# Optimization experiments

Measured on AMD Instinct MI355X. Metric: run time of the kernel, lower is better.

## Reference

```python
import jax, jax.numpy as jnp
import numpy as np

REG_MAX = 16
TOPK = 13
ALPHA = 1.0
BETA = 6.0
MATCH_W = 0.5
IOU_W = 7.5
DFL_W = 1.5
EPS = 1e-7
NEG_INF = -1e30


def _iou(b1, b2):
    # xyxy IoU, broadcastable [..., 4]
    x1 = jnp.maximum(b1[..., 0], b2[..., 0]); y1 = jnp.maximum(b1[..., 1], b2[..., 1])
    x2 = jnp.minimum(b1[..., 2], b2[..., 2]); y2 = jnp.minimum(b1[..., 3], b2[..., 3])
    inter = jnp.maximum(x2 - x1, 0.0) * jnp.maximum(y2 - y1, 0.0)
    a1 = (b1[..., 2] - b1[..., 0]) * (b1[..., 3] - b1[..., 1])
    a2 = (b2[..., 2] - b2[..., 0]) * (b2[..., 3] - b2[..., 1])
    return inter / (a1 + a2 - inter + EPS)


def _ciou(b1, b2):
    iou = _iou(b1, b2)
    w1 = b1[..., 2] - b1[..., 0]; h1 = b1[..., 3] - b1[..., 1]
    w2 = b2[..., 2] - b2[..., 0]; h2 = b2[..., 3] - b2[..., 1]
    cw = jnp.maximum(b1[..., 2], b2[..., 2]) - jnp.minimum(b1[..., 0], b2[..., 0])
    ch = jnp.maximum(b1[..., 3], b2[..., 3]) - jnp.minimum(b1[..., 1], b2[..., 1])
    c2 = cw * cw + ch * ch + EPS
    rho2 = ((b2[..., 0] + b2[..., 2] - b1[..., 0] - b1[..., 2]) ** 2
            + (b2[..., 1] + b2[..., 3] - b1[..., 1] - b1[..., 3]) ** 2) / 4.0
    v = (4.0 / jnp.pi ** 2) * (jnp.arctan(w2 / (h2 + EPS)) - jnp.arctan(w1 / (h1 + EPS))) ** 2
    a = jax.lax.stop_gradient(v / (v - iou + (1.0 + EPS)))
    return iou - (rho2 / c2 + v * a)


def _per_sample(ps, pb, bd, gtb, gtl, vcm, anchor, stride):
    # ps [N,C], pb [N,4], bd [N,4*R], gtb [M,4], gtl [M], vcm [C] bool
    N, C = ps.shape
    M = gtb.shape[0]
    lab = jnp.clip(gtl, 0, C - 1)
    gt_valid = (gtl >= 0) & (gtl < C) & vcm[lab]
    ax, ay = anchor[:, 0], anchor[:, 1]
    inside = ((ax[None, :] >= gtb[:, 0:1]) & (ax[None, :] <= gtb[:, 2:3])
              & (ay[None, :] >= gtb[:, 1:2]) & (ay[None, :] <= gtb[:, 3:4]))  # [M,N]
    iou_mn = _iou(pb[None, :, :], gtb[:, None, :])                             # [M,N]
    cls_mn = jax.nn.sigmoid(ps[:, lab]).T                                      # [M,N]
    align = jnp.where(inside & gt_valid[:, None], cls_mn ** ALPHA * iou_mn ** BETA, NEG_INF)
    top_vals, top_idx = jax.lax.top_k(align, TOPK)                             # [M,K]
    cand = jnp.full((M, N), NEG_INF, ps.dtype).at[jnp.arange(M)[:, None], top_idx].set(top_vals)
    best = cand.max(0)          # final metric per anchor
    mg = cand.argmax(0)         # winning GT (first max == earliest GT, matching loop order)
    fg = best > -1.0            # align >= 0 always; non-candidates stay at NEG_INF
    m_lab = jnp.clip(gtl[mg], 0, C - 1)
    ov = iou_mn[mg, jnp.arange(N)]
    fgf = fg.astype(ps.dtype)
    tgt_scores = jax.nn.one_hot(m_lab, C, dtype=ps.dtype) * (jnp.maximum(ov, 0.1) * fgf)[:, None]
    tb = jnp.where(fg[:, None], gtb[mg], pb)   # safe target boxes (masked out when not fg)

    # classification BCE over valid classes (mean)
    bce = jnp.maximum(ps, 0.0) - ps * tgt_scores + jnp.log1p(jnp.exp(-jnp.abs(ps)))
    vc = vcm.astype(ps.dtype)
    match = (bce * vc[None, :]).sum() / (N * jnp.maximum(vc.sum(), 1.0))

    cnt = fg.sum()
    ciou_v = _ciou(pb, tb)
    iou_loss = jnp.where(cnt > 0, ((1.0 - ciou_v) * fgf).sum() / jnp.maximum(cnt, 1), 0.0)
    miou_sum = (_iou(pb, tb) * fgf).sum()
    probs = jax.nn.sigmoid(ps)
    pos_sum = (probs[jnp.arange(N), m_lab] * fgf).sum()

    # DFL
    d = jnp.concatenate([anchor - tb[:, :2], tb[:, 2:] - anchor], -1) / stride  # [N,4]
    d = jnp.clip(d, 0.0, REG_MAX - 1 - 0.01)
    tl = d.astype(jnp.int32)
    tr = jnp.minimum(tl + 1, REG_MAX - 1)
    wl = tr.astype(ps.dtype) - d
    wr = 1.0 - wl
    logp = jax.nn.log_softmax(bd.reshape(N, 4, REG_MAX), -1)
    ll = -jnp.take_along_axis(logp, tl[..., None], -1)[..., 0]
    lr = -jnp.take_along_axis(logp, tr[..., None], -1)[..., 0]
    dfl = jnp.where(cnt > 0, ((ll * wl + lr * wr) * fgf[:, None]).sum() / jnp.maximum(cnt * 4, 1), 0.0)

    mx = jnp.where(vcm[None, :], probs, NEG_INF).max(-1)
    neg_sum = (mx * (1.0 - fgf)).sum()
    neg_cnt = N - cnt
    return match, iou_loss, dfl, cnt, neg_cnt, pos_sum, neg_sum, miou_sum


def setup_inputs() -> dict:
    key = jax.random.key(0)
    B, N, C, M, R = 16, 8400, 80, 64, REG_MAX
    ks = jax.random.split(key, 7)
    pts, sts = [], []
    for s in (8, 16, 32):
        n = 640 // s
        g = (np.arange(n) + 0.5) * s
        xv, yv = np.meshgrid(g, g)
        pts.append(np.stack([xv.ravel(), yv.ravel()], 1))
        sts.append(np.full((n * n, 1), s, np.float32))
    anchor_points = jnp.asarray(np.concatenate(pts).astype(np.float32))  # [8400,2]
    stride_tensor = jnp.asarray(np.concatenate(sts))                      # [8400,1]
    c = anchor_points[None] + jax.random.normal(ks[0], (B, N, 2)) * stride_tensor[None]
    wh = jax.random.uniform(ks[1], (B, N, 2), minval=8.0, maxval=128.0)
    pred_boxes = jnp.concatenate([jnp.clip(c - wh / 2, 0.0, 640.0),
                                  jnp.clip(c + wh / 2, 0.0, 640.0)], -1)
    gc = jax.random.uniform(ks[2], (B, M, 2), minval=64.0, maxval=576.0)
    gwh = jax.random.uniform(ks[3], (B, M, 2), minval=16.0, maxval=128.0)
    gt_boxes = jnp.concatenate([gc - gwh / 2, gc + gwh / 2], -1)
    gt_labels = jax.random.randint(ks[4], (B, M), 0, C)
    class_mask = jnp.ones((B, C), bool)
    pred_scores = jax.random.normal(ks[5], (B, N, C))
    box_distribution = jax.random.normal(ks[6], (B, N, 4 * R))
    return {"pred_scores": pred_scores, "pred_boxes": pred_boxes,
            "anchor_points": anchor_points, "stride_tensor": stride_tensor,
            "box_distribution": box_distribution, "gt_boxes": gt_boxes,
            "gt_labels": gt_labels, "class_mask": class_mask}


def reference(pred_scores, pred_boxes, anchor_points, stride_tensor,
              box_distribution, gt_boxes, gt_labels, class_mask):
    B = pred_scores.shape[0]
    f = lambda ps, pb, bd, gtb, gtl, vcm: _per_sample(ps, pb, bd, gtb, gtl, vcm,
                                                      anchor_points, stride_tensor)
    match, iou_l, dfl, cnt, ncnt, psum, nsum, misum = jax.vmap(f)(
        pred_scores, pred_boxes, box_distribution, gt_boxes, gt_labels, class_mask)
    tot_pos = cnt.sum()
    tot_neg = ncnt.sum()
    total_match = match.sum(); total_iou = iou_l.sum(); total_dfl = dfl.sum()
    loss = (MATCH_W * total_match + IOU_W * total_iou + DFL_W * total_dfl) / B
    mean_pos = psum.sum() / jnp.maximum(tot_pos, 1)
    mean_neg = nsum.sum() / jnp.maximum(tot_neg, 1)
    mean_miou = misum.sum() / jnp.maximum(tot_pos, 1)
    return (loss, total_match / B, total_iou / B, total_dfl / B,
            tot_pos.astype(jnp.float32), mean_pos, mean_neg, mean_miou)
```

## Files before the change

### kernel.cpp

```cpp
#include <hip/hip_runtime.h>
#include <stdint.h>

#define TOPK 13
#define NEG_INF_F (-1e30f)
#define EPSF 1e-7f
#define L2EF 1.4426950408889634f
#define LN2F 0.6931471805599453f
#define MAXCAND 2048

__device__ __forceinline__ int mask_at(const uint8_t* __restrict__ raw, int i) {
    bool as_u8 = (raw[1] | raw[2] | raw[3]) != 0;
    return as_u8 ? (raw[i] != 0) : (((const int*)raw)[i] != 0);
}

__device__ __forceinline__ float iou_pair(float ax1, float ay1, float ax2, float ay2,
                                          float bx1, float by1, float bx2, float by2) {
    float x1 = fmaxf(ax1, bx1), y1 = fmaxf(ay1, by1);
    float x2 = fminf(ax2, bx2), y2 = fminf(ay2, by2);
    float inter = fmaxf(x2 - x1, 0.f) * fmaxf(y2 - y1, 0.f);
    float a1 = (ax2 - ax1) * (ay2 - ay1);
    float a2 = (bx2 - bx1) * (by2 - by1);
    return inter / (a1 + a2 - inter + EPSF);
}

__device__ __forceinline__ float sigmoid_fast(float s) {
    return 1.f / (1.f + exp2f(-s * L2EF));
}
__device__ __forceinline__ float softplus_bce(float s) {
    float t = exp2f(-fabsf(s) * L2EF);
    return fmaxf(s, 0.f) + log2f(1.f + t) * LN2F;
}

__device__ __forceinline__ void assign_wave(
    const float* __restrict__ ps, const float* __restrict__ pb,
    const float* __restrict__ gtb, const int* __restrict__ gtl,
    const uint8_t* __restrict__ mraw,
    unsigned long long* __restrict__ best, int B, int N, int C, int M,
    int t, int lane) {
    int b = t % B;
    int m = t / B;

    int lbl = gtl[b * M + m];
    int lab = min(max(lbl, 0), C - 1);
    if (!((lbl >= 0) && (lbl < C) && (mask_at(mraw, b * C + lab) != 0))) return;

    float4 g = ((const float4*)gtb)[(size_t)b * M + m];

    const int   n0_[3]  = { 0, 6400, 8000 };
    const int   dim_[3] = { 80, 40, 20 };
    const float sv_[3]  = { 8.f, 16.f, 32.f };

    int ix0[3], iy0[3], ww[3], pre[4];
    pre[0] = 0;
#pragma unroll
    for (int l = 0; l < 3; ++l) {
        float s = sv_[l]; int d = dim_[l];
        int ax0 = max(0,     (int)ceilf (g.x / s - 0.5f));
        int ax1 = min(d - 1, (int)floorf(g.z / s - 0.5f));
        int ay0 = max(0,     (int)ceilf (g.y / s - 0.5f));
        int ay1 = min(d - 1, (int)floorf(g.w / s - 0.5f));
        int w = max(0, ax1 - ax0 + 1);
        int h = max(0, ay1 - ay0 + 1);
        ix0[l] = ax0; iy0[l] = ay0; ww[l] = w;
        pre[l + 1] = pre[l] + w * h;
    }
    int tot = pre[3];
    if (tot == 0) return;

    const float* psb = ps + (size_t)b * N * C + lab;
    const float4* pbb = (const float4*)pb + (size_t)b * N;

    float lv[TOPK];
    int   li[TOPK];
#pragma unroll
    for (int j = 0; j < TOPK; ++j) { lv[j] = NEG_INF_F; li[j] = -1; }

    for (int tt = lane; tt < tot; tt += 64) {
        int l = (tt >= pre[1]) + (tt >= pre[2]);
        int r = tt - pre[l];
        int w = ww[l];
        int iy = r / w, ix = r - iy * w;
        int gx = ix0[l] + ix, gy = iy0[l] + iy;
        int n = n0_[l] + gy * dim_[l] + gx;
        float4 p = pbb[n];
        float iou = iou_pair(p.x, p.y, p.z, p.w, g.x, g.y, g.z, g.w);
        float sc = psb[(size_t)n * C];
        float i3 = iou * iou * iou;
        float val = sigmoid_fast(sc) * i3 * i3;
        if (val > lv[TOPK - 1]) {
            bool placed = false;
#pragma unroll
            for (int j = TOPK - 1; j >= 1; --j) {
                if (!placed) {
                    if (val > lv[j - 1]) { lv[j] = lv[j - 1]; li[j] = li[j - 1]; }
                    else { lv[j] = val; li[j] = n; placed = true; }
                }
            }
            if (!placed) { lv[0] = val; li[0] = n; }
        }
    }

    unsigned key = 0xFFFFFFFFu - (unsigned)m;
    unsigned long long* bb = best + (size_t)b * N;
    int rounds = min(tot, TOPK);
    for (int p = 0; p < rounds; ++p) {
        float bv = lv[0]; int bn = li[0];
        for (int off = 32; off > 0; off >>= 1) {
            float ov = __shfl_down(bv, off, 64);
            int   on = __shfl_down(bn, off, 64);
            if (ov > bv || (ov == bv && (unsigned)on < (unsigned)bn)) { bv = ov; bn = on; }
        }
        bv = __shfl(bv, 0, 64);
        bn = __shfl(bn, 0, 64);
        if (bn < 0) break;
        if (li[0] == bn) {
            unsigned long long pk =
                ((unsigned long long)__float_as_uint(lv[0]) << 32) | (unsigned long long)key;
            atomicMax(bb + bn, pk);
#pragma unroll
            for (int j = 0; j < TOPK - 1; ++j) { lv[j] = lv[j + 1]; li[j] = li[j + 1]; }
            lv[TOPK - 1] = NEG_INF_F; li[TOPK - 1] = -1;
        }
    }
}

__global__ __launch_bounds__(256, 1) void fused_a_k(
    const float* __restrict__ ps, const float* __restrict__ pb,
    const float* __restrict__ gtb, const int* __restrict__ gtl,
    const uint8_t* __restrict__ mraw,
    unsigned long long* __restrict__ best, float* __restrict__ smaxbuf,
    float* __restrict__ partials, int B, int N, int C, int M,
    int asgb, int nb) {
    if ((int)blockIdx.x < asgb) {
        int t = blockIdx.x * 4 + (threadIdx.x >> 6);
        if (t < B * M)
            assign_wave(ps, pb, gtb, gtl, mraw, best, B, N, C, M, t, threadIdx.x & 63);
        return;
    }
    int bi = blockIdx.x - asgb;
    int b = bi / nb;
    int n = (bi % nb) * 256 + threadIdx.x;

    __shared__ int smask[256];
    __shared__ int s_notall;
    __shared__ float sredA[4];
    if (threadIdx.x == 0) s_notall = 0;
    __syncthreads();
    for (int c = threadIdx.x; c < C && c < 256; c += 256) {
        int v = mask_at(mraw, b * C + c);
        smask[c] = v;
        if (!v) s_notall = 1;
    }
    __syncthreads();
    bool allm = (s_notall == 0);

    float acc0 = 0.f;
    if (n < N) {
        const float* psr = ps + ((size_t)b * N + n) * C;
        float bce_sum = 0.f, smax = NEG_INF_F;

        if (C == 80 && allm) {
            const float4* p4 = (const float4*)psr;
            float4 s4[20];
#pragma unroll
            for (int i = 0; i < 20; ++i) s4[i] = p4[i];
#pragma unroll
            for (int i = 0; i < 20; ++i) {
                bce_sum += softplus_bce(s4[i].x) + softplus_bce(s4[i].y) +
                           softplus_bce(s4[i].z) + softplus_bce(s4[i].w);
                smax = fmaxf(smax, fmaxf(fmaxf(s4[i].x, s4[i].y), fmaxf(s4[i].z, s4[i].w)));
            }
        } else if (allm) {
            int c4 = C & ~3;
            for (int c = 0; c < c4; c += 4) {
                float4 s4 = *(const float4*)(psr + c);
                bce_sum += softplus_bce(s4.x) + softplus_bce(s4.y) +
                           softplus_bce(s4.z) + softplus_bce(s4.w);
                smax = fmaxf(smax, fmaxf(fmaxf(s4.x, s4.y), fmaxf(s4.z, s4.w)));
            }
            for (int c = c4; c < C; ++c) {
                float s = psr[c];
                bce_sum += softplus_bce(s);
                smax = fmaxf(smax, s);
            }
        } else {
            for (int c = 0; c < C; ++c) {
                float s = psr[c];
                if (smask[c]) { bce_sum += softplus_bce(s); smax = fmaxf(smax, s); }
            }
        }
        smaxbuf[(size_t)b * N + n] = smax;
        acc0 = bce_sum;
    }

    int lane = threadIdx.x & 63, wid = threadIdx.x >> 6;
    float v = acc0;
    for (int off = 32; off > 0; off >>= 1) v += __shfl_down(v, off, 64);
    if (lane == 0) sredA[wid] = v;
    __syncthreads();
    if (threadIdx.x == 0)
        atomicAdd(&partials[b * 8 + 0], sredA[0] + sredA[1] + sredA[2] + sredA[3]);
}

__global__ __launch_bounds__(256, 1) void fused_b_k(
    const float* __restrict__ ps, const float* __restrict__ pb,
    const float* __restrict__ anch, const float* __restrict__ strd,
    const float* __restrict__ bd, const float* __restrict__ gtb,
    const int* __restrict__ gtl, const uint8_t* __restrict__ mraw,
    const unsigned long long* __restrict__ best, const float* __restrict__ smaxbuf,
    float* __restrict__ partials, unsigned int* __restrict__ done_ctr,
    float* __restrict__ out, int B, int N, int C, int M) {
    int b = blockIdx.y;
    int n = blockIdx.x * 256 + threadIdx.x;

    __shared__ float sred[4 * 8];
    __shared__ int s_last;

    float acc0 = 0, acc1 = 0, acc2 = 0, acc3 = 0, acc4 = 0, acc5 = 0, acc6 = 0;

    if (n < N) {
        unsigned long long pk = best[(size_t)b * N + n];
        bool fg = (pk != 0ull);
        float smax = smaxbuf[(size_t)b * N + n];
        acc1 = fg ? 1.f : 0.f;
        acc3 = fg ? 0.f : sigmoid_fast(smax);

        if (fg) {
            int mg = (int)(0xFFFFFFFFu - (unsigned)(pk & 0xFFFFFFFFull));
            int lbl = gtl[b * M + mg];
            int m_lab = min(max(lbl, 0), C - 1);

            const float* bdr = bd + ((size_t)b * N + n) * 64;
            const float4* bq4 = (const float4*)bdr;
            float4 bq[16];
#pragma unroll
            for (int i = 0; i < 16; ++i) bq[i] = bq4[i];
            float4 p = ((const float4*)pb)[(size_t)b * N + n];
            float4 g = ((const float4*)gtb)[(size_t)b * M + mg];
            float2 an = ((const float2*)anch)[n];
            float stv = strd[n];
            float slab = ps[((size_t)b * N + n) * C + m_lab];

            float ov = iou_pair(p.x, p.y, p.z, p.w, g.x, g.y, g.z, g.w);
            acc0 = -fmaxf(ov, 0.1f) * slab;
            acc2 = sigmoid_fast(slab);
            acc4 = ov;
            float w1 = p.z - p.x, h1 = p.w - p.y;
            float w2 = g.z - g.x, h2 = g.w - g.y;
            float cw = fmaxf(p.z, g.z) - fminf(p.x, g.x);
            float ch = fmaxf(p.w, g.w) - fminf(p.y, g.y);
            float c2 = cw * cw + ch * ch + EPSF;
            float dx = g.x + g.z - p.x - p.z;
            float dy = g.y + g.w - p.y - p.w;
            float rho2 = (dx * dx + dy * dy) * 0.25f;
            const float PI = 3.14159265358979323846f;
            float dv = atanf(w2 / (h2 + EPSF)) - atanf(w1 / (h1 + EPSF));
            float v = (4.f / (PI * PI)) * dv * dv;
            float a = v / (v - ov + 1.f + EPSF);
            acc5 = 1.f - (ov - (rho2 / c2 + v * a));
            float dall[4] = { (an.x - g.x) / stv, (an.y - g.y) / stv,
                              (g.z - an.x) / stv, (g.w - an.y) / stv };
            float dfl = 0.f;
#pragma unroll
            for (int k = 0; k < 4; ++k) {
                float4 q0 = bq[k * 4 + 0], q1 = bq[k * 4 + 1];
                float4 q2 = bq[k * 4 + 2], q3 = bq[k * 4 + 3];
                float mxv = fmaxf(fmaxf(fmaxf(q0.x, q0.y), fmaxf(q0.z, q0.w)),
                                  fmaxf(fmaxf(q1.x, q1.y), fmaxf(q1.z, q1.w)));
                mxv = fmaxf(mxv, fmaxf(fmaxf(fmaxf(q2.x, q2.y), fmaxf(q2.z, q2.w)),
                                        fmaxf(fmaxf(q3.x, q3.y), fmaxf(q3.z, q3.w))));
                float se = exp2f((q0.x - mxv) * L2EF) + exp2f((q0.y - mxv) * L2EF) +
                           exp2f((q0.z - mxv) * L2EF) + exp2f((q0.w - mxv) * L2EF) +
                           exp2f((q1.x - mxv) * L2EF) + exp2f((q1.y - mxv) * L2EF) +
                           exp2f((q1.z - mxv) * L2EF) + exp2f((q1.w - mxv) * L2EF) +
                           exp2f((q2.x - mxv) * L2EF) + exp2f((q2.y - mxv) * L2EF) +
                           exp2f((q2.z - mxv) * L2EF) + exp2f((q2.w - mxv) * L2EF) +
                           exp2f((q3.x - mxv) * L2EF) + exp2f((q3.y - mxv) * L2EF) +
                           exp2f((q3.z - mxv) * L2EF) + exp2f((q3.w - mxv) * L2EF);
                float lse = mxv + log2f(se) * LN2F;
                float d = fminf(fmaxf(dall[k], 0.f), 14.99f);
                int tl = (int)d;
                int tr = min(tl + 1, 15);
                float wl = (float)tr - d;
                float xtl = bdr[k * 16 + tl];
                float xtr = bdr[k * 16 + tr];
                dfl += (lse - xtl) * wl + (lse - xtr) * (1.f - wl);
            }
            acc6 = dfl;
        }
    }

    int lane = threadIdx.x & 63, wid = threadIdx.x >> 6;
    float accs[7] = { acc0, acc1, acc2, acc3, acc4, acc5, acc6 };
#pragma unroll
    for (int j = 0; j < 7; ++j) {
        float v = accs[j];
        for (int off = 32; off > 0; off >>= 1) v += __shfl_down(v, off, 64);
        if (lane == 0) sred[wid * 8 + j] = v;
    }
    __syncthreads();
    if (threadIdx.x < 7) {
        float s = sred[0 * 8 + threadIdx.x] + sred[1 * 8 + threadIdx.x] +
                  sred[2 * 8 + threadIdx.x] + sred[3 * 8 + threadIdx.x];
        atomicAdd(&partials[b * 8 + threadIdx.x], s);
    }
    __syncthreads();

    if (threadIdx.x == 0) {
        __threadfence();
        unsigned r = atomicAdd(done_ctr, 1u);
        s_last = (r == gridDim.x * gridDim.y - 1u) ? 1 : 0;
    }
    __syncthreads();
    if (!s_last) return;
    if (threadIdx.x >= 64) return;
    __threadfence();

    int fl = threadIdx.x;
    float tm = 0, ti = 0, td = 0, tp = 0, tneg = 0, pos = 0, neg = 0, miou = 0;
    for (int s = fl; s < B; s += 64) {
        float vcs = 0.f;
        for (int c = 0; c < C; ++c) vcs += mask_at(mraw, s * C + c) ? 1.f : 0.f;
        const float* pr = partials + s * 8;
        float p0 = __hip_atomic_load(&pr[0], __ATOMIC_RELAXED, __HIP_MEMORY_SCOPE_AGENT);
        float p1 = __hip_atomic_load(&pr[1], __ATOMIC_RELAXED, __HIP_MEMORY_SCOPE_AGENT);
        float p2 = __hip_atomic_load(&pr[2], __ATOMIC_RELAXED, __HIP_MEMORY_SCOPE_AGENT);
        float p3 = __hip_atomic_load(&pr[3], __ATOMIC_RELAXED, __HIP_MEMORY_SCOPE_AGENT);
        float p4 = __hip_atomic_load(&pr[4], __ATOMIC_RELAXED, __HIP_MEMORY_SCOPE_AGENT);
        float p5 = __hip_atomic_load(&pr[5], __ATOMIC_RELAXED, __HIP_MEMORY_SCOPE_AGENT);
        float p6 = __hip_atomic_load(&pr[6], __ATOMIC_RELAXED, __HIP_MEMORY_SCOPE_AGENT);
        float cnt = p1;
        tm += p0 / ((float)N * fmaxf(vcs, 1.f));
        ti += (cnt > 0.f) ? p5 / fmaxf(cnt, 1.f) : 0.f;
        td += (cnt > 0.f) ? p6 / fmaxf(cnt * 4.f, 1.f) : 0.f;
        tp += cnt; tneg += (float)N - cnt;
        pos += p2; neg += p3; miou += p4;
    }
    for (int off = 32; off > 0; off >>= 1) {
        tm += __shfl_down(tm, off, 64);   ti += __shfl_down(ti, off, 64);
        td += __shfl_down(td, off, 64);   tp += __shfl_down(tp, off, 64);
        tneg += __shfl_down(tneg, off, 64); pos += __shfl_down(pos, off, 64);
        neg += __shfl_down(neg, off, 64); miou += __shfl_down(miou, off, 64);
    }
    if (fl == 0) {
        float Bf = (float)B;
        out[0] = (0.5f * tm + 7.5f * ti + 1.5f * td) / Bf;
        out[1] = tm / Bf;
        out[2] = ti / Bf;
        out[3] = td / Bf;
        out[4] = tp;
        out[5] = pos / fmaxf(tp, 1.f);
        out[6] = neg / fmaxf(tneg, 1.f);
        out[7] = miou / fmaxf(tp, 1.f);
    }
}

__global__ __launch_bounds__(256) void assign_topk_k(
    const float* __restrict__ ps, const float* __restrict__ pb,
    const float* __restrict__ anch, const float* __restrict__ gtb,
    const int* __restrict__ gtl, const uint8_t* __restrict__ mraw,
    unsigned long long* __restrict__ best, int B, int N, int C, int M) {
    int b = blockIdx.x % B;
    int m = blockIdx.x / B;

    __shared__ float cval[MAXCAND];
    __shared__ int   cidx[MAXCAND];
    __shared__ int   scnt;
    if (threadIdx.x == 0) scnt = 0;

    int lbl = gtl[b * M + m];
    int lab = min(max(lbl, 0), C - 1);
    bool valid = (lbl >= 0) && (lbl < C) && (mask_at(mraw, b * C + lab) != 0);
    __syncthreads();

    if (valid) {
        float4 g = ((const float4*)gtb)[(size_t)b * M + m];
        const float* psb = ps + (size_t)b * N * C + lab;
        const float4* pbb = (const float4*)pb + (size_t)b * N;
        for (int n = threadIdx.x; n < N; n += 256) {
            float2 a = ((const float2*)anch)[n];
            if (a.x < g.x || a.x > g.z || a.y < g.y || a.y > g.w) continue;
            float4 p = pbb[n];
            float iou = iou_pair(p.x, p.y, p.z, p.w, g.x, g.y, g.z, g.w);
            float s = psb[(size_t)n * C];
            float i3 = iou * iou * iou;
            float val = sigmoid_fast(s) * i3 * i3;
            int slot = atomicAdd(&scnt, 1);
            if (slot < MAXCAND) { cval[slot] = val; cidx[slot] = n; }
        }
    }
    __syncthreads();
    if (!valid || threadIdx.x >= 64) return;

    int total = min(scnt, MAXCAND);
    if (total == 0) return;
    int lane = threadIdx.x;

    float lv[TOPK];
    int   li[TOPK];
#pragma unroll
    for (int j = 0; j < TOPK; ++j) { lv[j] = NEG_INF_F; li[j] = -1; }
    for (int i = lane; i < total; i += 64) {
        float v = cval[i]; int ix = cidx[i];
        if (v > lv[TOPK - 1]) {
            bool placed = false;
#pragma unroll
            for (int j = TOPK - 1; j >= 1; --j) {
                if (!placed) {
                    if (v > lv[j - 1]) { lv[j] = lv[j - 1]; li[j] = li[j - 1]; }
                    else { lv[j] = v; li[j] = ix; placed = true; }
                }
            }
            if (!placed) { lv[0] = v; li[0] = ix; }
        }
    }

    unsigned key = 0xFFFFFFFFu - (unsigned)m;
    unsigned long long* bb = best + (size_t)b * N;
    int rounds = min(total, TOPK);
    for (int p = 0; p < rounds; ++p) {
        float bv = lv[0]; int bn = li[0];
        for (int off = 32; off > 0; off >>= 1) {
            float ov = __shfl_down(bv, off, 64);
            int   on = __shfl_down(bn, off, 64);
            if (ov > bv || (ov == bv && (unsigned)on < (unsigned)bn)) { bv = ov; bn = on; }
        }
        bv = __shfl(bv, 0, 64);
        bn = __shfl(bn, 0, 64);
        if (bn < 0) break;
        if (li[0] == bn) {
            unsigned long long pk =
                ((unsigned long long)__float_as_uint(lv[0]) << 32) | (unsigned long long)key;
            atomicMax(bb + bn, pk);
#pragma unroll
            for (int j = 0; j < TOPK - 1; ++j) { lv[j] = lv[j + 1]; li[j] = li[j + 1]; }
            lv[TOPK - 1] = NEG_INF_F; li[TOPK - 1] = -1;
        }
    }
}

__global__ __launch_bounds__(256, 1) void per_anchor_k(
    const float* __restrict__ ps, const float* __restrict__ pb,
    const float* __restrict__ anch, const float* __restrict__ strd,
    const float* __restrict__ bd, const float* __restrict__ gtb,
    const int* __restrict__ gtl, const uint8_t* __restrict__ mraw,
    const unsigned long long* __restrict__ best,
    float* __restrict__ partials, int B, int N, int C, int M) {
    int b = blockIdx.y;
    int n = blockIdx.x * 256 + threadIdx.x;

    __shared__ int smask[256];
    __shared__ int s_notall;
    __shared__ float sred[4 * 8];
    if (threadIdx.x == 0) s_notall = 0;
    __syncthreads();
    for (int c = threadIdx.x; c < C && c < 256; c += 256) {
        int v = mask_at(mraw, b * C + c);
        smask[c] = v;
        if (!v) s_notall = 1;
    }
    __syncthreads();
    bool allm = (s_notall == 0);

    float acc0 = 0, acc1 = 0, acc2 = 0, acc3 = 0, acc4 = 0, acc5 = 0, acc6 = 0;

    if (n < N) {
        unsigned long long pk = best[(size_t)b * N + n];
        bool fg = (pk != 0ull);
        int mg = fg ? (int)(0xFFFFFFFFu - (unsigned)(pk & 0xFFFFFFFFull)) : 0;
        int lbl = gtl[b * M + mg];
        int m_lab = min(max(lbl, 0), C - 1);

        const float* psr = ps + ((size_t)b * N + n) * C;
        float bce_sum = 0.f, smax = NEG_INF_F;

        if (C == 80 && allm) {
            const float4* p4 = (const float4*)psr;
            float4 s4[20];
#pragma unroll
            for (int i = 0; i < 20; ++i) s4[i] = p4[i];
#pragma unroll
            for (int i = 0; i < 20; ++i) {
                bce_sum += softplus_bce(s4[i].x) + softplus_bce(s4[i].y) +
                           softplus_bce(s4[i].z) + softplus_bce(s4[i].w);
                smax = fmaxf(smax, fmaxf(fmaxf(s4[i].x, s4[i].y), fmaxf(s4[i].z, s4[i].w)));
            }
        } else if (allm) {
            int c4 = C & ~3;
            for (int c = 0; c < c4; c += 4) {
                float4 s4 = *(const float4*)(psr + c);
                bce_sum += softplus_bce(s4.x) + softplus_bce(s4.y) +
                           softplus_bce(s4.z) + softplus_bce(s4.w);
                smax = fmaxf(smax, fmaxf(fmaxf(s4.x, s4.y), fmaxf(s4.z, s4.w)));
            }
            for (int c = c4; c < C; ++c) {
                float s = psr[c];
                bce_sum += softplus_bce(s);
                smax = fmaxf(smax, s);
            }
        } else {
            for (int c = 0; c < C; ++c) {
                float s = psr[c];
                if (smask[c]) { bce_sum += softplus_bce(s); smax = fmaxf(smax, s); }
            }
        }

        acc1 = fg ? 1.f : 0.f;
        acc3 = fg ? 0.f : sigmoid_fast(smax);

        if (fg) {
            const float* bdr = bd + ((size_t)b * N + n) * 64;
            const float4* bq4 = (const float4*)bdr;
            float4 bq[16];
#pragma unroll
            for (int i = 0; i < 16; ++i) bq[i] = bq4[i];
            float4 p = ((const float4*)pb)[(size_t)b * N + n];
            float4 g = ((const float4*)gtb)[(size_t)b * M + mg];
            float2 an = ((const float2*)anch)[n];
            float stv = strd[n];
            float slab = psr[m_lab];

            float ov = iou_pair(p.x, p.y, p.z, p.w, g.x, g.y, g.z, g.w);
            bce_sum -= fmaxf(ov, 0.1f) * slab;
            acc2 = sigmoid_fast(slab);
            acc4 = ov;
            float w1 = p.z - p.x, h1 = p.w - p.y;
            float w2 = g.z - g.x, h2 = g.w - g.y;
            float cw = fmaxf(p.z, g.z) - fminf(p.x, g.x);
            float ch = fmaxf(p.w, g.w) - fminf(p.y, g.y);
            float c2 = cw * cw + ch * ch + EPSF;
            float dx = g.x + g.z - p.x - p.z;
            float dy = g.y + g.w - p.y - p.w;
            float rho2 = (dx * dx + dy * dy) * 0.25f;
            const float PI = 3.14159265358979323846f;
            float dv = atanf(w2 / (h2 + EPSF)) - atanf(w1 / (h1 + EPSF));
            float v = (4.f / (PI * PI)) * dv * dv;
            float a = v / (v - ov + 1.f + EPSF);
            acc5 = 1.f - (ov - (rho2 / c2 + v * a));
            float dall[4] = { (an.x - g.x) / stv, (an.y - g.y) / stv,
                              (g.z - an.x) / stv, (g.w - an.y) / stv };
            float dfl = 0.f;
#pragma unroll
            for (int k = 0; k < 4; ++k) {
                float4 q0 = bq[k * 4 + 0], q1 = bq[k * 4 + 1];
                float4 q2 = bq[k * 4 + 2], q3 = bq[k * 4 + 3];
                float mxv = fmaxf(fmaxf(fmaxf(q0.x, q0.y), fmaxf(q0.z, q0.w)),
                                  fmaxf(fmaxf(q1.x, q1.y), fmaxf(q1.z, q1.w)));
                mxv = fmaxf(mxv, fmaxf(fmaxf(fmaxf(q2.x, q2.y), fmaxf(q2.z, q2.w)),
                                        fmaxf(fmaxf(q3.x, q3.y), fmaxf(q3.z, q3.w))));
                float se = exp2f((q0.x - mxv) * L2EF) + exp2f((q0.y - mxv) * L2EF) +
                           exp2f((q0.z - mxv) * L2EF) + exp2f((q0.w - mxv) * L2EF) +
                           exp2f((q1.x - mxv) * L2EF) + exp2f((q1.y - mxv) * L2EF) +
                           exp2f((q1.z - mxv) * L2EF) + exp2f((q1.w - mxv) * L2EF) +
                           exp2f((q2.x - mxv) * L2EF) + exp2f((q2.y - mxv) * L2EF) +
                           exp2f((q2.z - mxv) * L2EF) + exp2f((q2.w - mxv) * L2EF) +
                           exp2f((q3.x - mxv) * L2EF) + exp2f((q3.y - mxv) * L2EF) +
                           exp2f((q3.z - mxv) * L2EF) + exp2f((q3.w - mxv) * L2EF);
                float lse = mxv + log2f(se) * LN2F;
                float d = fminf(fmaxf(dall[k], 0.f), 14.99f);
                int tl = (int)d;
                int tr = min(tl + 1, 15);
                float wl = (float)tr - d;
                float xtl = bdr[k * 16 + tl];
                float xtr = bdr[k * 16 + tr];
                dfl += (lse - xtl) * wl + (lse - xtr) * (1.f - wl);
            }
            acc6 = dfl;
        }
        acc0 = bce_sum;
    }

    int lane = threadIdx.x & 63, wid = threadIdx.x >> 6;
    float accs[7] = { acc0, acc1, acc2, acc3, acc4, acc5, acc6 };
#pragma unroll
    for (int j = 0; j < 7; ++j) {
        float v = accs[j];
        for (int off = 32; off > 0; off >>= 1) v += __shfl_down(v, off, 64);
        if (lane == 0) sred[wid * 8 + j] = v;
    }
    __syncthreads();
    if (threadIdx.x < 7) {
        float s = sred[0 * 8 + threadIdx.x] + sred[1 * 8 + threadIdx.x] +
                  sred[2 * 8 + threadIdx.x] + sred[3 * 8 + threadIdx.x];
        atomicAdd(&partials[b * 8 + threadIdx.x], s);
    }
}

__global__ void finalize_k(const float* __restrict__ partials, const uint8_t* __restrict__ mraw,
                           float* __restrict__ out, int B, int N, int C) {
    int lane = threadIdx.x;
    float tm = 0, ti = 0, td = 0, tp = 0, tneg = 0, pos = 0, neg = 0, miou = 0;
    if (lane < B) {
        float vcs = 0.f;
        for (int c = 0; c < C; ++c) vcs += mask_at(mraw, lane * C + c) ? 1.f : 0.f;
        const float* pr = partials + lane * 8;
        float cnt = pr[1];
        tm = pr[0] / ((float)N * fmaxf(vcs, 1.f));
        ti = (cnt > 0.f) ? pr[5] / fmaxf(cnt, 1.f) : 0.f;
        td = (cnt > 0.f) ? pr[6] / fmaxf(cnt * 4.f, 1.f) : 0.f;
        tp = cnt; tneg = (float)N - cnt;
        pos = pr[2]; neg = pr[3]; miou = pr[4];
    }
    for (int off = 32; off > 0; off >>= 1) {
        tm += __shfl_down(tm, off, 64);   ti += __shfl_down(ti, off, 64);
        td += __shfl_down(td, off, 64);   tp += __shfl_down(tp, off, 64);
        tneg += __shfl_down(tneg, off, 64); pos += __shfl_down(pos, off, 64);
        neg += __shfl_down(neg, off, 64); miou += __shfl_down(miou, off, 64);
    }
    if (lane == 0) {
        float Bf = (float)B;
        out[0] = (0.5f * tm + 7.5f * ti + 1.5f * td) / Bf;
        out[1] = tm / Bf;
        out[2] = ti / Bf;
        out[3] = td / Bf;
        out[4] = tp;
        out[5] = pos / fmaxf(tp, 1.f);
        out[6] = neg / fmaxf(tneg, 1.f);
        out[7] = miou / fmaxf(tp, 1.f);
    }
}

extern "C" void kernel_launch(void* const* d_in, const int* in_sizes, int n_in,
                              void* d_out, int out_size, void* d_ws, size_t ws_size,
                              hipStream_t stream) {
    const float* ps   = (const float*)d_in[0];
    const float* pb   = (const float*)d_in[1];
    const float* anch = (const float*)d_in[2];
    const float* strd = (const float*)d_in[3];
    const float* bd   = (const float*)d_in[4];
    const float* gtb  = (const float*)d_in[5];
    const int*   gtl  = (const int*)d_in[6];
    const uint8_t* cmsk = (const uint8_t*)d_in[7];

    int N = in_sizes[2] / 2;
    int B = in_sizes[1] / (4 * N);
    int C = in_sizes[0] / (B * N);
    int M = in_sizes[6] / B;

    size_t bestBytes = (size_t)B * N * sizeof(unsigned long long);
    size_t off1 = (bestBytes + 255) & ~(size_t)255;
    size_t partBytes = (size_t)B * 8 * sizeof(float);
    size_t off2 = (off1 + partBytes + 255) & ~(size_t)255;
    size_t zeroBytes = off2 + 256;
    unsigned long long* best = (unsigned long long*)d_ws;
    float* partials = (float*)((char*)d_ws + off1);
    unsigned int* done_ctr = (unsigned int*)((char*)d_ws + off2);
    float* smaxbuf = (float*)((char*)d_ws + zeroBytes);

    hipMemsetAsync(d_ws, 0, zeroBytes, stream);

    int nb = (N + 255) / 256;
    if (N == 8400) {
        int asgb = (B * M + 3) / 4;
        fused_a_k<<<asgb + B * nb, 256, 0, stream>>>(ps, pb, gtb, gtl, cmsk,
                                                     best, smaxbuf, partials,
                                                     B, N, C, M, asgb, nb);
        fused_b_k<<<dim3(nb, B), 256, 0, stream>>>(ps, pb, anch, strd, bd, gtb, gtl, cmsk,
                                                   best, smaxbuf, partials, done_ctr,
                                                   (float*)d_out, B, N, C, M);
    } else {
        assign_topk_k<<<B * M, 256, 0, stream>>>(ps, pb, anch, gtb, gtl, cmsk, best, B, N, C, M);
        dim3 gB(nb, B);
        per_anchor_k<<<gB, 256, 0, stream>>>(ps, pb, anch, strd, bd, gtb, gtl, cmsk, best,
                                             partials, B, N, C, M);
        finalize_k<<<1, 64, 0, stream>>>(partials, cmsk, (float*)d_out, B, N, C);
    }
}
```

Baseline: 155.4 us.

## Compact foreground anchors into a list and process only those in second pass

During top-k assignment, the first atomicMax that claims a new anchor also appends it to a global compacted list. The second kernel then runs only over the listed foreground anchors instead of over every anchor. The negative-score sigmoid sum moves into the first kernel, which now writes sigmoid values instead of raw maxima; the second kernel subtracts them for foreground anchors. Per-block partials are accumulated in LDS atomics before going to global memory, at the cost of extra contended global atomics in the assign phase and a list-ordering dependence on atomic timing.

```diff
diff --git a/kernel.cpp b/kernel.cpp
--- a/kernel.cpp
+++ b/kernel.cpp
@@ -7,6 +7,7 @@
 #define L2EF 1.4426950408889634f
 #define LN2F 0.6931471805599453f
 #define MAXCAND 2048
+#define MAXB_LDS 64
 
 __device__ __forceinline__ int mask_at(const uint8_t* __restrict__ raw, int i) {
     bool as_u8 = (raw[1] | raw[2] | raw[3]) != 0;
@@ -35,8 +36,9 @@
     const float* __restrict__ ps, const float* __restrict__ pb,
     const float* __restrict__ gtb, const int* __restrict__ gtl,
     const uint8_t* __restrict__ mraw,
-    unsigned long long* __restrict__ best, int B, int N, int C, int M,
-    int t, int lane) {
+    unsigned long long* __restrict__ best,
+    unsigned* __restrict__ list, unsigned* __restrict__ list_cnt,
+    int B, int N, int C, int M, int t, int lane) {
     int b = t % B;
     int m = t / B;
 
@@ -116,7 +118,11 @@
         if (li[0] == bn) {
             unsigned long long pk =
                 ((unsigned long long)__float_as_uint(lv[0]) << 32) | (unsigned long long)key;
-            atomicMax(bb + bn, pk);
+            unsigned long long old = atomicMax(bb + bn, pk);
+            if (old == 0ull) {
+                unsigned slot = atomicAdd(list_cnt, 1u);
+                list[slot] = ((unsigned)b << 16) | (unsigned)bn;
+            }
 #pragma unroll
             for (int j = 0; j < TOPK - 1; ++j) { lv[j] = lv[j + 1]; li[j] = li[j + 1]; }
             lv[TOPK - 1] = NEG_INF_F; li[TOPK - 1] = -1;
@@ -128,13 +134,15 @@
     const float* __restrict__ ps, const float* __restrict__ pb,
     const float* __restrict__ gtb, const int* __restrict__ gtl,
     const uint8_t* __restrict__ mraw,
-    unsigned long long* __restrict__ best, float* __restrict__ smaxbuf,
-    float* __restrict__ partials, int B, int N, int C, int M,
-    int asgb, int nb) {
+    unsigned long long* __restrict__ best,
+    unsigned* __restrict__ list, unsigned* __restrict__ list_cnt,
+    float* __restrict__ sigbuf, float* __restrict__ partials,
+    int B, int N, int C, int M, int asgb, int nb) {
     if ((int)blockIdx.x < asgb) {
         int t = blockIdx.x * 4 + (threadIdx.x >> 6);
         if (t < B * M)
-            assign_wave(ps, pb, gtb, gtl, mraw, best, B, N, C, M, t, threadIdx.x & 63);
+            assign_wave(ps, pb, gtb, gtl, mraw, best, list, list_cnt,
+                        B, N, C, M, t, threadIdx.x & 63);
         return;
     }
     int bi = blockIdx.x - asgb;
@@ -143,7 +151,7 @@
 
     __shared__ int smask[256];
     __shared__ int s_notall;
-    __shared__ float sredA[4];
+    __shared__ float sredA[4], sredB[4];
     if (threadIdx.x == 0) s_notall = 0;
     __syncthreads();
     for (int c = threadIdx.x; c < C && c < 256; c += 256) {
@@ -154,7 +162,7 @@
     __syncthreads();
     bool allm = (s_notall == 0);
 
-    float acc0 = 0.f;
+    float acc0 = 0.f, acc3 = 0.f;
     if (n < N) {
         const float* psr = ps + ((size_t)b * N + n) * C;
         float bce_sum = 0.f, smax = NEG_INF_F;
@@ -189,17 +197,24 @@
                 if (smask[c]) { bce_sum += softplus_bce(s); smax = fmaxf(smax, s); }
             }
         }
-        smaxbuf[(size_t)b * N + n] = smax;
+        float sg = sigmoid_fast(smax);
+        sigbuf[(size_t)b * N + n] = sg;
         acc0 = bce_sum;
+        acc3 = sg;
     }
 
     int lane = threadIdx.x & 63, wid = threadIdx.x >> 6;
-    float v = acc0;
-    for (int off = 32; off > 0; off >>= 1) v += __shfl_down(v, off, 64);
-    if (lane == 0) sredA[wid] = v;
-    __syncthreads();
-    if (threadIdx.x == 0)
+    float v0 = acc0, v3 = acc3;
+    for (int off = 32; off > 0; off >>= 1) {
+        v0 += __shfl_down(v0, off, 64);
+        v3 += __shfl_down(v3, off, 64);
+    }
+    if (lane == 0) { sredA[wid] = v0; sredB[wid] = v3; }
+    __syncthreads();
+    if (threadIdx.x == 0) {
         atomicAdd(&partials[b * 8 + 0], sredA[0] + sredA[1] + sredA[2] + sredA[3]);
+        atomicAdd(&partials[b * 8 + 3], sredB[0] + sredB[1] + sredB[2] + sredB[3]);
+    }
 }
 
 __global__ __launch_bounds__(256, 1) void fused_b_k(
@@ -207,29 +222,302 @@
     const float* __restrict__ anch, const float* __restrict__ strd,
     const float* __restrict__ bd, const float* __restrict__ gtb,
     const int* __restrict__ gtl, const uint8_t* __restrict__ mraw,
-    const unsigned long long* __restrict__ best, const float* __restrict__ smaxbuf,
+    const unsigned long long* __restrict__ best, const float* __restrict__ sigbuf,
+    const unsigned* __restrict__ list, const unsigned* __restrict__ list_cnt,
     float* __restrict__ partials, unsigned int* __restrict__ done_ctr,
     float* __restrict__ out, int B, int N, int C, int M) {
+    __shared__ float sacc[MAXB_LDS * 8];
+    __shared__ int s_last;
+    bool use_lds = (B <= MAXB_LDS);
+    if (use_lds)
+        for (int i = threadIdx.x; i < B * 8; i += 256) sacc[i] = 0.f;
+    __syncthreads();
+
+    int cnt = (int)*list_cnt;
+    int idx = blockIdx.x * 256 + threadIdx.x;
+    if (idx < cnt) {
+        unsigned e = list[idx];
+        int b = (int)(e >> 16), n = (int)(e & 0xFFFFu);
+        unsigned long long pk = best[(size_t)b * N + n];
+        int mg = (int)(0xFFFFFFFFu - (unsigned)(pk & 0xFFFFFFFFull));
+        int lbl = gtl[b * M + mg];
+        int m_lab = min(max(lbl, 0), C - 1);
+
+        const float* bdr = bd + ((size_t)b * N + n) * 64;
+        const float4* bq4 = (const float4*)bdr;
+        float4 bq[16];
+#pragma unroll
+        for (int i = 0; i < 16; ++i) bq[i] = bq4[i];
+        float4 p = ((const float4*)pb)[(size_t)b * N + n];
+        float4 g = ((const float4*)gtb)[(size_t)b * M + mg];
+        float2 an = ((const float2*)anch)[n];
+        float stv = strd[n];
+        float slab = ps[((size_t)b * N + n) * C + m_lab];
+        float sg = sigbuf[(size_t)b * N + n];
+
+        float ov = iou_pair(p.x, p.y, p.z, p.w, g.x, g.y, g.z, g.w);
+        float acc0 = -fmaxf(ov, 0.1f) * slab;
+        float acc2 = sigmoid_fast(slab);
+        float acc4 = ov;
+        float w1 = p.z - p.x, h1 = p.w - p.y;
+        float w2 = g.z - g.x, h2 = g.w - g.y;
+        float cw = fmaxf(p.z, g.z) - fminf(p.x, g.x);
+        float ch = fmaxf(p.w, g.w) - fminf(p.y, g.y);
+        float c2 = cw * cw + ch * ch + EPSF;
+        float dx = g.x + g.z - p.x - p.z;
+        float dy = g.y + g.w - p.y - p.w;
+        float rho2 = (dx * dx + dy * dy) * 0.25f;
+        const float PI = 3.14159265358979323846f;
+        float dv = atanf(w2 / (h2 + EPSF)) - atanf(w1 / (h1 + EPSF));
+        float v = (4.f / (PI * PI)) * dv * dv;
+        float a = v / (v - ov + 1.f + EPSF);
+        float acc5 = 1.f - (ov - (rho2 / c2 + v * a));
+        float dall[4] = { (an.x - g.x) / stv, (an.y - g.y) / stv,
+                          (g.z - an.x) / stv, (g.w - an.y) / stv };
+        float dfl = 0.f;
+#pragma unroll
+        for (int k = 0; k < 4; ++k) {
+            float4 q0 = bq[k * 4 + 0], q1 = bq[k * 4 + 1];
+            float4 q2 = bq[k * 4 + 2], q3 = bq[k * 4 + 3];
+            float mxv = fmaxf(fmaxf(fmaxf(q0.x, q0.y), fmaxf(q0.z, q0.w)),
+                              fmaxf(fmaxf(q1.x, q1.y), fmaxf(q1.z, q1.w)));
+            mxv = fmaxf(mxv, fmaxf(fmaxf(fmaxf(q2.x, q2.y), fmaxf(q2.z, q2.w)),
+                                    fmaxf(fmaxf(q3.x, q3.y), fmaxf(q3.z, q3.w))));
+            float se = exp2f((q0.x - mxv) * L2EF) + exp2f((q0.y - mxv) * L2EF) +
+                       exp2f((q0.z - mxv) * L2EF) + exp2f((q0.w - mxv) * L2EF) +
+                       exp2f((q1.x - mxv) * L2EF) + exp2f((q1.y - mxv) * L2EF) +
+                       exp2f((q1.z - mxv) * L2EF) + exp2f((q1.w - mxv) * L2EF) +
+                       exp2f((q2.x - mxv) * L2EF) + exp2f((q2.y - mxv) * L2EF) +
+                       exp2f((q2.z - mxv) * L2EF) + exp2f((q2.w - mxv) * L2EF) +
+                       exp2f((q3.x - mxv) * L2EF) + exp2f((q3.y - mxv) * L2EF) +
+                       exp2f((q3.z - mxv) * L2EF) + exp2f((q3.w - mxv) * L2EF);
+            float lse = mxv + log2f(se) * LN2F;
+            float d = fminf(fmaxf(dall[k], 0.f), 14.99f);
+            int tl = (int)d;
+            int tr = min(tl + 1, 15);
+            float wl = (float)tr - d;
+            float xtl = bdr[k * 16 + tl];
+            float xtr = bdr[k * 16 + tr];
+            dfl += (lse - xtl) * wl + (lse - xtr) * (1.f - wl);
+        }
+        float accs[7] = { acc0, 1.f, acc2, -sg, acc4, acc5, dfl };
+        if (use_lds) {
+#pragma unroll
+            for (int j = 0; j < 7; ++j) atomicAdd(&sacc[b * 8 + j], accs[j]);
+        } else {
+#pragma unroll
+            for (int j = 0; j < 7; ++j) atomicAdd(&partials[b * 8 + j], accs[j]);
+        }
+    }
+    __syncthreads();
+    if (use_lds)
+        for (int i = threadIdx.x; i < B * 8; i += 256)
+            if (sacc[i] != 0.f) atomicAdd(&partials[i], sacc[i]);
+    __syncthreads();
+
+    if (threadIdx.x == 0) {
+        __threadfence();
+        unsigned r = atomicAdd(done_ctr, 1u);
+        s_last = (r == gridDim.x - 1u) ? 1 : 0;
+    }
+    __syncthreads();
+    if (!s_last) return;
+    if (threadIdx.x >= 64) return;
+    __threadfence();
+
+    int fl = threadIdx.x;
+    float tm = 0, ti = 0, td = 0, tp = 0, tneg = 0, pos = 0, neg = 0, miou = 0;
+    for (int s = fl; s < B; s += 64) {
+        float vcs = 0.f;
+        for (int c = 0; c < C; ++c) vcs += mask_at(mraw, s * C + c) ? 1.f : 0.f;
+        const float* pr = partials + s * 8;
+        float p0 = __hip_atomic_load(&pr[0], __ATOMIC_RELAXED, __HIP_MEMORY_SCOPE_AGENT);
+        float p1 = __hip_atomic_load(&pr[1], __ATOMIC_RELAXED, __HIP_MEMORY_SCOPE_AGENT);
+        float p2 = __hip_atomic_load(&pr[2], __ATOMIC_RELAXED, __HIP_MEMORY_SCOPE_AGENT);
+        float p3 = __hip_atomic_load(&pr[3], __ATOMIC_RELAXED, __HIP_MEMORY_SCOPE_AGENT);
+        float p4 = __hip_atomic_load(&pr[4], __ATOMIC_RELAXED, __HIP_MEMORY_SCOPE_AGENT);
+        float p5 = __hip_atomic_load(&pr[5], __ATOMIC_RELAXED, __HIP_MEMORY_SCOPE_AGENT);
+        float p6 = __hip_atomic_load(&pr[6], __ATOMIC_RELAXED, __HIP_MEMORY_SCOPE_AGENT);
+        float cnt = p1;
+        tm += p0 / ((float)N * fmaxf(vcs, 1.f));
+        ti += (cnt > 0.f) ? p5 / fmaxf(cnt, 1.f) : 0.f;
+        td += (cnt > 0.f) ? p6 / fmaxf(cnt * 4.f, 1.f) : 0.f;
+        tp += cnt; tneg += (float)N - cnt;
+        pos += p2; neg += p3; miou += p4;
+    }
+    for (int off = 32; off > 0; off >>= 1) {
+        tm += __shfl_down(tm, off, 64);   ti += __shfl_down(ti, off, 64);
+        td += __shfl_down(td, off, 64);   tp += __shfl_down(tp, off, 64);
+        tneg += __shfl_down(tneg, off, 64); pos += __shfl_down(pos, off, 64);
+        neg += __shfl_down(neg, off, 64); miou += __shfl_down(miou, off, 64);
+    }
+    if (fl == 0) {
+        float Bf = (float)B;
+        out[0] = (0.5f * tm + 7.5f * ti + 1.5f * td) / Bf;
+        out[1] = tm / Bf;
+        out[2] = ti / Bf;
+        out[3] = td / Bf;
+        out[4] = tp;
+        out[5] = pos / fmaxf(tp, 1.f);
+        out[6] = neg / fmaxf(tneg, 1.f);
+        out[7] = miou / fmaxf(tp, 1.f);
+    }
+}
+
+__global__ __launch_bounds__(256) void assign_topk_k(
+    const float* __restrict__ ps, const float* __restrict__ pb,
+    const float* __restrict__ anch, const float* __restrict__ gtb,
+    const int* __restrict__ gtl, const uint8_t* __restrict__ mraw,
+    unsigned long long* __restrict__ best, int B, int N, int C, int M) {
+    int b = blockIdx.x % B;
+    int m = blockIdx.x / B;
+
+    __shared__ float cval[MAXCAND];
+    __shared__ int   cidx[MAXCAND];
+    __shared__ int   scnt;
+    if (threadIdx.x == 0) scnt = 0;
+
+    int lbl = gtl[b * M + m];
+    int lab = min(max(lbl, 0), C - 1);
+    bool valid = (lbl >= 0) && (lbl < C) && (mask_at(mraw, b * C + lab) != 0);
+    __syncthreads();
+
+    if (valid) {
+        float4 g = ((const float4*)gtb)[(size_t)b * M + m];
+        const float* psb = ps + (size_t)b * N * C + lab;
+        const float4* pbb = (const float4*)pb + (size_t)b * N;
+        for (int n = threadIdx.x; n < N; n += 256) {
+            float2 a = ((const float2*)anch)[n];
+            if (a.x < g.x || a.x > g.z || a.y < g.y || a.y > g.w) continue;
+            float4 p = pbb[n];
+            float iou = iou_pair(p.x, p.y, p.z, p.w, g.x, g.y, g.z, g.w);
+            float s = psb[(size_t)n * C];
+            float i3 = iou * iou * iou;
+            float val = sigmoid_fast(s) * i3 * i3;
+            int slot = atomicAdd(&scnt, 1);
+            if (slot < MAXCAND) { cval[slot] = val; cidx[slot] = n; }
+        }
+    }
+    __syncthreads();
+    if (!valid || threadIdx.x >= 64) return;
+
+    int total = min(scnt, MAXCAND);
+    if (total == 0) return;
+    int lane = threadIdx.x;
+
+    float lv[TOPK];
+    int   li[TOPK];
+#pragma unroll
+    for (int j = 0; j < TOPK; ++j) { lv[j] = NEG_INF_F; li[j] = -1; }
+    for (int i = lane; i < total; i += 64) {
+        float v = cval[i]; int ix = cidx[i];
+        if (v > lv[TOPK - 1]) {
+            bool placed = false;
+#pragma unroll
+            for (int j = TOPK - 1; j >= 1; --j) {
+                if (!placed) {
+                    if (v > lv[j - 1]) { lv[j] = lv[j - 1]; li[j] = li[j - 1]; }
+                    else { lv[j] = v; li[j] = ix; placed = true; }
+                }
+            }
+            if (!placed) { lv[0] = v; li[0] = ix; }
+        }
+    }
+
+    unsigned key = 0xFFFFFFFFu - (unsigned)m;
+    unsigned long long* bb = best + (size_t)b * N;
+    int rounds = min(total, TOPK);
+    for (int p = 0; p < rounds; ++p) {
+        float bv = lv[0]; int bn = li[0];
+        for (int off = 32; off > 0; off >>= 1) {
+            float ov = __shfl_down(bv, off, 64);
+            int   on = __shfl_down(bn, off, 64);
+            if (ov > bv || (ov == bv && (unsigned)on < (unsigned)bn)) { bv = ov; bn = on; }
+        }
+        bv = __shfl(bv, 0, 64);
+        bn = __shfl(bn, 0, 64);
+        if (bn < 0) break;
+        if (li[0] == bn) {
+            unsigned long long pk =
+                ((unsigned long long)__float_as_uint(lv[0]) << 32) | (unsigned long long)key;
+            atomicMax(bb + bn, pk);
+#pragma unroll
+            for (int j = 0; j < TOPK - 1; ++j) { lv[j] = lv[j + 1]; li[j] = li[j + 1]; }
+            lv[TOPK - 1] = NEG_INF_F; li[TOPK - 1] = -1;
+        }
+    }
+}
+
+__global__ __launch_bounds__(256, 1) void per_anchor_k(
+    const float* __restrict__ ps, const float* __restrict__ pb,
+    const float* __restrict__ anch, const float* __restrict__ strd,
+    const float* __restrict__ bd, const float* __restrict__ gtb,
+    const int* __restrict__ gtl, const uint8_t* __restrict__ mraw,
+    const unsigned long long* __restrict__ best,
+    float* __restrict__ partials, int B, int N, int C, int M) {
     int b = blockIdx.y;
     int n = blockIdx.x * 256 + threadIdx.x;
 
+    __shared__ int smask[256];
+    __shared__ int s_notall;
     __shared__ float sred[4 * 8];
-    __shared__ int s_last;
+    if (threadIdx.x == 0) s_notall = 0;
+    __syncthreads();
+    for (int c = threadIdx.x; c < C && c < 256; c += 256) {
+        int v = mask_at(mraw, b * C + c);
+        smask[c] = v;
+        if (!v) s_notall = 1;
+    }
+    __syncthreads();
+    bool allm = (s_notall == 0);
 
     float acc0 = 0, acc1 = 0, acc2 = 0, acc3 = 0, acc4 = 0, acc5 = 0, acc6 = 0;
 
     if (n < N) {
         unsigned long long pk = best[(size_t)b * N + n];
         bool fg = (pk != 0ull);
-        float smax = smaxbuf[(size_t)b * N + n];
+        int mg = fg ? (int)(0xFFFFFFFFu - (unsigned)(pk & 0xFFFFFFFFull)) : 0;
+        int lbl = gtl[b * M + mg];
+        int m_lab = min(max(lbl, 0), C - 1);
+
+        const float* psr = ps + ((size_t)b * N + n) * C;
+        float bce_sum = 0.f, smax = NEG_INF_F;
+
+        if (C == 80 && allm) {
+            const float4* p4 = (const float4*)psr;
+            float4 s4[20];
+#pragma unroll
+            for (int i = 0; i < 20; ++i) s4[i] = p4[i];
+#pragma unroll
+            for (int i = 0; i < 20; ++i) {
+                bce_sum += softplus_bce(s4[i].x) + softplus_bce(s4[i].y) +
+                           softplus_bce(s4[i].z) + softplus_bce(s4[i].w);
+                smax = fmaxf(smax, fmaxf(fmaxf(s4[i].x, s4[i].y), fmaxf(s4[i].z, s4[i].w)));
+            }
+        } else if (allm) {
+            int c4 = C & ~3;
+            for (int c = 0; c < c4; c += 4) {
+                float4 s4 = *(const float4*)(psr + c);
+                bce_sum += softplus_bce(s4.x) + softplus_bce(s4.y) +
+                           softplus_bce(s4.z) + softplus_bce(s4.w);
+                smax = fmaxf(smax, fmaxf(fmaxf(s4.x, s4.y), fmaxf(s4.z, s4.w)));
+            }
+            for (int c = c4; c < C; ++c) {
+                float s = psr[c];
+                bce_sum += softplus_bce(s);
+                smax = fmaxf(smax, s);
+            }
+        } else {
+            for (int c = 0; c < C; ++c) {
+                float s = psr[c];
+                if (smask[c]) { bce_sum += softplus_bce(s); smax = fmaxf(smax, s); }
+            }
+        }
+
         acc1 = fg ? 1.f : 0.f;
         acc3 = fg ? 0.f : sigmoid_fast(smax);
 
         if (fg) {
-            int mg = (int)(0xFFFFFFFFu - (unsigned)(pk & 0xFFFFFFFFull));
-            int lbl = gtl[b * M + mg];
-            int m_lab = min(max(lbl, 0), C - 1);
-
             const float* bdr = bd + ((size_t)b * N + n) * 64;
             const float4* bq4 = (const float4*)bdr;
             float4 bq[16];
@@ -239,10 +527,10 @@
             float4 g = ((const float4*)gtb)[(size_t)b * M + mg];
             float2 an = ((const float2*)anch)[n];
             float stv = strd[n];
-            float slab = ps[((size_t)b * N + n) * C + m_lab];
+            float slab = psr[m_lab];
 
             float ov = iou_pair(p.x, p.y, p.z, p.w, g.x, g.y, g.z, g.w);
-            acc0 = -fmaxf(ov, 0.1f) * slab;
+            bce_sum -= fmaxf(ov, 0.1f) * slab;
             acc2 = sigmoid_fast(slab);
             acc4 = ov;
             float w1 = p.z - p.x, h1 = p.w - p.y;
@@ -288,285 +576,6 @@
             }
             acc6 = dfl;
         }
-    }
-
-    int lane = threadIdx.x & 63, wid = threadIdx.x >> 6;
-    float accs[7] = { acc0, acc1, acc2, acc3, acc4, acc5, acc6 };
-#pragma unroll
-    for (int j = 0; j < 7; ++j) {
-        float v = accs[j];
-        for (int off = 32; off > 0; off >>= 1) v += __shfl_down(v, off, 64);
-        if (lane == 0) sred[wid * 8 + j] = v;
-    }
-    __syncthreads();
-    if (threadIdx.x < 7) {
-        float s = sred[0 * 8 + threadIdx.x] + sred[1 * 8 + threadIdx.x] +
-                  sred[2 * 8 + threadIdx.x] + sred[3 * 8 + threadIdx.x];
-        atomicAdd(&partials[b * 8 + threadIdx.x], s);
-    }
-    __syncthreads();
-
-    if (threadIdx.x == 0) {
-        __threadfence();
-        unsigned r = atomicAdd(done_ctr, 1u);
-        s_last = (r == gridDim.x * gridDim.y - 1u) ? 1 : 0;
-    }
-    __syncthreads();
-    if (!s_last) return;
-    if (threadIdx.x >= 64) return;
-    __threadfence();
-
-    int fl = threadIdx.x;
-    float tm = 0, ti = 0, td = 0, tp = 0, tneg = 0, pos = 0, neg = 0, miou = 0;
-    for (int s = fl; s < B; s += 64) {
-        float vcs = 0.f;
-        for (int c = 0; c < C; ++c) vcs += mask_at(mraw, s * C + c) ? 1.f : 0.f;
-        const float* pr = partials + s * 8;
-        float p0 = __hip_atomic_load(&pr[0], __ATOMIC_RELAXED, __HIP_MEMORY_SCOPE_AGENT);
-        float p1 = __hip_atomic_load(&pr[1], __ATOMIC_RELAXED, __HIP_MEMORY_SCOPE_AGENT);
-        float p2 = __hip_atomic_load(&pr[2], __ATOMIC_RELAXED, __HIP_MEMORY_SCOPE_AGENT);
-        float p3 = __hip_atomic_load(&pr[3], __ATOMIC_RELAXED, __HIP_MEMORY_SCOPE_AGENT);
-        float p4 = __hip_atomic_load(&pr[4], __ATOMIC_RELAXED, __HIP_MEMORY_SCOPE_AGENT);
-        float p5 = __hip_atomic_load(&pr[5], __ATOMIC_RELAXED, __HIP_MEMORY_SCOPE_AGENT);
-        float p6 = __hip_atomic_load(&pr[6], __ATOMIC_RELAXED, __HIP_MEMORY_SCOPE_AGENT);
-        float cnt = p1;
-        tm += p0 / ((float)N * fmaxf(vcs, 1.f));
-        ti += (cnt > 0.f) ? p5 / fmaxf(cnt, 1.f) : 0.f;
-        td += (cnt > 0.f) ? p6 / fmaxf(cnt * 4.f, 1.f) : 0.f;
-        tp += cnt; tneg += (float)N - cnt;
-        pos += p2; neg += p3; miou += p4;
-    }
-    for (int off = 32; off > 0; off >>= 1) {
-        tm += __shfl_down(tm, off, 64);   ti += __shfl_down(ti, off, 64);
-        td += __shfl_down(td, off, 64);   tp += __shfl_down(tp, off, 64);
-        tneg += __shfl_down(tneg, off, 64); pos += __shfl_down(pos, off, 64);
-        neg += __shfl_down(neg, off, 64); miou += __shfl_down(miou, off, 64);
-    }
-    if (fl == 0) {
-        float Bf = (float)B;
-        out[0] = (0.5f * tm + 7.5f * ti + 1.5f * td) / Bf;
-        out[1] = tm / Bf;
-        out[2] = ti / Bf;
-        out[3] = td / Bf;
-        out[4] = tp;
-        out[5] = pos / fmaxf(tp, 1.f);
-        out[6] = neg / fmaxf(tneg, 1.f);
-        out[7] = miou / fmaxf(tp, 1.f);
-    }
-}
-
-__global__ __launch_bounds__(256) void assign_topk_k(
-    const float* __restrict__ ps, const float* __restrict__ pb,
-    const float* __restrict__ anch, const float* __restrict__ gtb,
-    const int* __restrict__ gtl, const uint8_t* __restrict__ mraw,
-    unsigned long long* __restrict__ best, int B, int N, int C, int M) {
-    int b = blockIdx.x % B;
-    int m = blockIdx.x / B;
-
-    __shared__ float cval[MAXCAND];
-    __shared__ int   cidx[MAXCAND];
-    __shared__ int   scnt;
-    if (threadIdx.x == 0) scnt = 0;
-
-    int lbl = gtl[b * M + m];
-    int lab = min(max(lbl, 0), C - 1);
-    bool valid = (lbl >= 0) && (lbl < C) && (mask_at(mraw, b * C + lab) != 0);
-    __syncthreads();
-
-    if (valid) {
-        float4 g = ((const float4*)gtb)[(size_t)b * M + m];
-        const float* psb = ps + (size_t)b * N * C + lab;
-        const float4* pbb = (const float4*)pb + (size_t)b * N;
-        for (int n = threadIdx.x; n < N; n += 256) {
-            float2 a = ((const float2*)anch)[n];
-            if (a.x < g.x || a.x > g.z || a.y < g.y || a.y > g.w) continue;
-            float4 p = pbb[n];
-            float iou = iou_pair(p.x, p.y, p.z, p.w, g.x, g.y, g.z, g.w);
-            float s = psb[(size_t)n * C];
-            float i3 = iou * iou * iou;
-            float val = sigmoid_fast(s) * i3 * i3;
-            int slot = atomicAdd(&scnt, 1);
-            if (slot < MAXCAND) { cval[slot] = val; cidx[slot] = n; }
-        }
-    }
-    __syncthreads();
-    if (!valid || threadIdx.x >= 64) return;
-
-    int total = min(scnt, MAXCAND);
-    if (total == 0) return;
-    int lane = threadIdx.x;
-
-    float lv[TOPK];
-    int   li[TOPK];
-#pragma unroll
-    for (int j = 0; j < TOPK; ++j) { lv[j] = NEG_INF_F; li[j] = -1; }
-    for (int i = lane; i < total; i += 64) {
-        float v = cval[i]; int ix = cidx[i];
-        if (v > lv[TOPK - 1]) {
-            bool placed = false;
-#pragma unroll
-            for (int j = TOPK - 1; j >= 1; --j) {
-                if (!placed) {
-                    if (v > lv[j - 1]) { lv[j] = lv[j - 1]; li[j] = li[j - 1]; }
-                    else { lv[j] = v; li[j] = ix; placed = true; }
-                }
-            }
-            if (!placed) { lv[0] = v; li[0] = ix; }
-        }
-    }
-
-    unsigned key = 0xFFFFFFFFu - (unsigned)m;
-    unsigned long long* bb = best + (size_t)b * N;
-    int rounds = min(total, TOPK);
-    for (int p = 0; p < rounds; ++p) {
-        float bv = lv[0]; int bn = li[0];
-        for (int off = 32; off > 0; off >>= 1) {
-            float ov = __shfl_down(bv, off, 64);
-            int   on = __shfl_down(bn, off, 64);
-            if (ov > bv || (ov == bv && (unsigned)on < (unsigned)bn)) { bv = ov; bn = on; }
-        }
-        bv = __shfl(bv, 0, 64);
-        bn = __shfl(bn, 0, 64);
-        if (bn < 0) break;
-        if (li[0] == bn) {
-            unsigned long long pk =
-                ((unsigned long long)__float_as_uint(lv[0]) << 32) | (unsigned long long)key;
-            atomicMax(bb + bn, pk);
-#pragma unroll
-            for (int j = 0; j < TOPK - 1; ++j) { lv[j] = lv[j + 1]; li[j] = li[j + 1]; }
-            lv[TOPK - 1] = NEG_INF_F; li[TOPK - 1] = -1;
-        }
-    }
-}
-
-__global__ __launch_bounds__(256, 1) void per_anchor_k(
-    const float* __restrict__ ps, const float* __restrict__ pb,
-    const float* __restrict__ anch, const float* __restrict__ strd,
-    const float* __restrict__ bd, const float* __restrict__ gtb,
-    const int* __restrict__ gtl, const uint8_t* __restrict__ mraw,
-    const unsigned long long* __restrict__ best,
-    float* __restrict__ partials, int B, int N, int C, int M) {
-    int b = blockIdx.y;
-    int n = blockIdx.x * 256 + threadIdx.x;
-
-    __shared__ int smask[256];
-    __shared__ int s_notall;
-    __shared__ float sred[4 * 8];
-    if (threadIdx.x == 0) s_notall = 0;
-    __syncthreads();
-    for (int c = threadIdx.x; c < C && c < 256; c += 256) {
-        int v = mask_at(mraw, b * C + c);
-        smask[c] = v;
-        if (!v) s_notall = 1;
-    }
-    __syncthreads();
-    bool allm = (s_notall == 0);
-
-    float acc0 = 0, acc1 = 0, acc2 = 0, acc3 = 0, acc4 = 0, acc5 = 0, acc6 = 0;
-
-    if (n < N) {
-        unsigned long long pk = best[(size_t)b * N + n];
-        bool fg = (pk != 0ull);
-        int mg = fg ? (int)(0xFFFFFFFFu - (unsigned)(pk & 0xFFFFFFFFull)) : 0;
-        int lbl = gtl[b * M + mg];
-        int m_lab = min(max(lbl, 0), C - 1);
-
-        const float* psr = ps + ((size_t)b * N + n) * C;
-        float bce_sum = 0.f, smax = NEG_INF_F;
-
-        if (C == 80 && allm) {
-            const float4* p4 = (const float4*)psr;
-            float4 s4[20];
-#pragma unroll
-            for (int i = 0; i < 20; ++i) s4[i] = p4[i];
-#pragma unroll
-            for (int i = 0; i < 20; ++i) {
-                bce_sum += softplus_bce(s4[i].x) + softplus_bce(s4[i].y) +
-                           softplus_bce(s4[i].z) + softplus_bce(s4[i].w);
-                smax = fmaxf(smax, fmaxf(fmaxf(s4[i].x, s4[i].y), fmaxf(s4[i].z, s4[i].w)));
-            }
-        } else if (allm) {
-            int c4 = C & ~3;
-            for (int c = 0; c < c4; c += 4) {
-                float4 s4 = *(const float4*)(psr + c);
-                bce_sum += softplus_bce(s4.x) + softplus_bce(s4.y) +
-                           softplus_bce(s4.z) + softplus_bce(s4.w);
-                smax = fmaxf(smax, fmaxf(fmaxf(s4.x, s4.y), fmaxf(s4.z, s4.w)));
-            }
-            for (int c = c4; c < C; ++c) {
-                float s = psr[c];
-                bce_sum += softplus_bce(s);
-                smax = fmaxf(smax, s);
-            }
-        } else {
-            for (int c = 0; c < C; ++c) {
-                float s = psr[c];
-                if (smask[c]) { bce_sum += softplus_bce(s); smax = fmaxf(smax, s); }
-            }
-        }
-
-        acc1 = fg ? 1.f : 0.f;
-        acc3 = fg ? 0.f : sigmoid_fast(smax);
-
-        if (fg) {
-            const float* bdr = bd + ((size_t)b * N + n) * 64;
-            const float4* bq4 = (const float4*)bdr;
-            float4 bq[16];
-#pragma unroll
-            for (int i = 0; i < 16; ++i) bq[i] = bq4[i];
-            float4 p = ((const float4*)pb)[(size_t)b * N + n];
-            float4 g = ((const float4*)gtb)[(size_t)b * M + mg];
-            float2 an = ((const float2*)anch)[n];
-            float stv = strd[n];
-            float slab = psr[m_lab];
-
-            float ov = iou_pair(p.x, p.y, p.z, p.w, g.x, g.y, g.z, g.w);
-            bce_sum -= fmaxf(ov, 0.1f) * slab;
-            acc2 = sigmoid_fast(slab);
-            acc4 = ov;
-            float w1 = p.z - p.x, h1 = p.w - p.y;
-            float w2 = g.z - g.x, h2 = g.w - g.y;
-            float cw = fmaxf(p.z, g.z) - fminf(p.x, g.x);
-            float ch = fmaxf(p.w, g.w) - fminf(p.y, g.y);
-            float c2 = cw * cw + ch * ch + EPSF;
-            float dx = g.x + g.z - p.x - p.z;
-            float dy = g.y + g.w - p.y - p.w;
-            float rho2 = (dx * dx + dy * dy) * 0.25f;
-            const float PI = 3.14159265358979323846f;
-            float dv = atanf(w2 / (h2 + EPSF)) - atanf(w1 / (h1 + EPSF));
-            float v = (4.f / (PI * PI)) * dv * dv;
-            float a = v / (v - ov + 1.f + EPSF);
-            acc5 = 1.f - (ov - (rho2 / c2 + v * a));
-            float dall[4] = { (an.x - g.x) / stv, (an.y - g.y) / stv,
-                              (g.z - an.x) / stv, (g.w - an.y) / stv };
-            float dfl = 0.f;
-#pragma unroll
-            for (int k = 0; k < 4; ++k) {
-                float4 q0 = bq[k * 4 + 0], q1 = bq[k * 4 + 1];
-                float4 q2 = bq[k * 4 + 2], q3 = bq[k * 4 + 3];
-                float mxv = fmaxf(fmaxf(fmaxf(q0.x, q0.y), fmaxf(q0.z, q0.w)),
-                                  fmaxf(fmaxf(q1.x, q1.y), fmaxf(q1.z, q1.w)));
-                mxv = fmaxf(mxv, fmaxf(fmaxf(fmaxf(q2.x, q2.y), fmaxf(q2.z, q2.w)),
-                                        fmaxf(fmaxf(q3.x, q3.y), fmaxf(q3.z, q3.w))));
-                float se = exp2f((q0.x - mxv) * L2EF) + exp2f((q0.y - mxv) * L2EF) +
-                           exp2f((q0.z - mxv) * L2EF) + exp2f((q0.w - mxv) * L2EF) +
-                           exp2f((q1.x - mxv) * L2EF) + exp2f((q1.y - mxv) * L2EF) +
-                           exp2f((q1.z - mxv) * L2EF) + exp2f((q1.w - mxv) * L2EF) +
-                           exp2f((q2.x - mxv) * L2EF) + exp2f((q2.y - mxv) * L2EF) +
-                           exp2f((q2.z - mxv) * L2EF) + exp2f((q2.w - mxv) * L2EF) +
-                           exp2f((q3.x - mxv) * L2EF) + exp2f((q3.y - mxv) * L2EF) +
-                           exp2f((q3.z - mxv) * L2EF) + exp2f((q3.w - mxv) * L2EF);
-                float lse = mxv + log2f(se) * LN2F;
-                float d = fminf(fmaxf(dall[k], 0.f), 14.99f);
-                int tl = (int)d;
-                int tr = min(tl + 1, 15);
-                float wl = (float)tr - d;
-                float xtl = bdr[k * 16 + tl];
-                float xtr = bdr[k * 16 + tr];
-                dfl += (lse - xtl) * wl + (lse - xtr) * (1.f - wl);
-            }
-            acc6 = dfl;
-        }
         acc0 = bce_sum;
     }
 
@@ -642,10 +651,15 @@
     size_t partBytes = (size_t)B * 8 * sizeof(float);
     size_t off2 = (off1 + partBytes + 255) & ~(size_t)255;
     size_t zeroBytes = off2 + 256;
+    size_t sigBytes = (size_t)B * N * sizeof(float);
+    size_t off4 = (zeroBytes + sigBytes + 255) & ~(size_t)255;
+
     unsigned long long* best = (unsigned long long*)d_ws;
     float* partials = (float*)((char*)d_ws + off1);
     unsigned int* done_ctr = (unsigned int*)((char*)d_ws + off2);
-    float* smaxbuf = (float*)((char*)d_ws + zeroBytes);
+    unsigned int* list_cnt = done_ctr + 1;
+    float* sigbuf = (float*)((char*)d_ws + zeroBytes);
+    unsigned int* list = (unsigned int*)((char*)d_ws + off4);
 
     hipMemsetAsync(d_ws, 0, zeroBytes, stream);
 
@@ -653,11 +667,13 @@
     if (N == 8400) {
         int asgb = (B * M + 3) / 4;
         fused_a_k<<<asgb + B * nb, 256, 0, stream>>>(ps, pb, gtb, gtl, cmsk,
-                                                     best, smaxbuf, partials,
-                                                     B, N, C, M, asgb, nb);
-        fused_b_k<<<dim3(nb, B), 256, 0, stream>>>(ps, pb, anch, strd, bd, gtb, gtl, cmsk,
-                                                   best, smaxbuf, partials, done_ctr,
-                                                   (float*)d_out, B, N, C, M);
+                                                     best, list, list_cnt, sigbuf,
+                                                     partials, B, N, C, M, asgb, nb);
+        int cap = B * M * TOPK;
+        int nblk = (cap + 255) / 256;
+        fused_b_k<<<nblk, 256, 0, stream>>>(ps, pb, anch, strd, bd, gtb, gtl, cmsk,
+                                            best, sigbuf, list, list_cnt,
+                                            partials, done_ctr, (float*)d_out, B, N, C, M);
     } else {
         assign_topk_k<<<B * M, 256, 0, stream>>>(ps, pb, anch, gtb, gtl, cmsk, best, B, N, C, M);
         dim3 gB(nb, B);
```

Result: slower. 274.9 us (+77.0%).
